# Performance work log

Hardware: AMD Instinct MI355X
Metric: run time of the kernel (lower is better)

Reference implementation:

```python
import jax, jax.numpy as jnp
import numpy as np

N_NODES = 50000
N_EDGES = 800000
IN_DIM, HID_DIM, EMB_DIM = 128, 256, 64


def setup_inputs() -> dict:
    key = jax.random.key(0)
    ks = jax.random.split(key, 10)
    x = jax.random.normal(ks[0], (N_NODES, IN_DIM), dtype=jnp.float32)
    edge_index = jax.random.randint(ks[1], (2, N_EDGES), 0, N_NODES, dtype=jnp.int64)
    def glorot(k, fan_in, fan_out):
        s = jnp.sqrt(6.0 / (fan_in + fan_out))
        return jax.random.uniform(k, (fan_in, fan_out), jnp.float32, -s, s)
    return {
        "x": x,
        "edge_index": edge_index,
        "W1": glorot(ks[2], IN_DIM, HID_DIM), "b1": jnp.zeros((HID_DIM,), jnp.float32),
        "W2": glorot(ks[3], HID_DIM, EMB_DIM), "b2": jnp.zeros((EMB_DIM,), jnp.float32),
        "W3": glorot(ks[4], EMB_DIM, HID_DIM), "b3": jnp.zeros((HID_DIM,), jnp.float32),
        "W4": glorot(ks[5], HID_DIM, IN_DIM), "b4": jnp.zeros((IN_DIM,), jnp.float32),
    }


def _gcn_conv(x, W, b, src, dst, norm, n_nodes):
    # linear transform, then edge gather -> normalize -> scatter-add (PyG GCNConv)
    h = x @ W                                    # [N, out]
    msg = h[src] * norm[:, None]                 # [E+N, out]
    out = jax.ops.segment_sum(msg, dst, num_segments=n_nodes)
    return out + b


def reference(x, edge_index, W1, b1, W2, b2, W3, b3, W4, b4):
    n = x.shape[0]
    loops = jnp.arange(n, dtype=edge_index.dtype)
    src = jnp.concatenate([edge_index[0], loops])  # add self-loops
    dst = jnp.concatenate([edge_index[1], loops])
    # symmetric degree normalization: deg computed on destination incl. self-loops
    deg = jax.ops.segment_sum(jnp.ones_like(dst, dtype=x.dtype), dst, num_segments=n)
    dis = jax.lax.rsqrt(jnp.maximum(deg, 1.0))
    norm = dis[src] * dis[dst]                   # [E+N]

    h = jax.nn.relu(_gcn_conv(x, W1, b1, src, dst, norm, n))
    h = jax.nn.relu(_gcn_conv(h, W2, b2, src, dst, norm, n))
    h = jax.nn.relu(_gcn_conv(h, W3, b3, src, dst, norm, n))
    out = _gcn_conv(h, W4, b4, src, dst, norm, n)
    return out
```

## Files before the change

### kernel.cpp

```cpp
#include <hip/hip_runtime.h>

#define N_NODES 50000
#define N_EDGES 800000

static inline size_t align256(size_t x) { return (x + 255) & ~(size_t)255; }

typedef _Float16 f16x8 __attribute__((ext_vector_type(8)));
typedef float f32x4 __attribute__((ext_vector_type(4)));
typedef float f32x8 __attribute__((ext_vector_type(8)));


__global__ void count_kernel(const int* __restrict__ dst, int* __restrict__ counts,
                             int* __restrict__ rank, int E) {
    int e = blockIdx.x * blockDim.x + threadIdx.x;
    if (e < E) rank[e] = atomicAdd(&counts[dst[e]], 1);
}

__global__ void scan1_kernel(const int* __restrict__ counts, int* __restrict__ row_ptr,
                             int* __restrict__ bsum, int n) {
    __shared__ int sd[1024];
    int i = blockIdx.x * 1024 + threadIdx.x;
    int v = (i < n) ? counts[i] : 0;
    sd[threadIdx.x] = v;
    __syncthreads();
    #pragma unroll
    for (int off = 1; off < 1024; off <<= 1) {
        int t = 0;
        if ((int)threadIdx.x >= off) t = sd[threadIdx.x - off];
        __syncthreads();
        sd[threadIdx.x] += t;
        __syncthreads();
    }
    if (i < n) row_ptr[i + 1] = sd[threadIdx.x];
    if (threadIdx.x == 1023) bsum[blockIdx.x] = sd[1023];
}

__global__ void scan3_kernel(int* __restrict__ row_ptr, const int* __restrict__ bsum,
                             const int* __restrict__ counts, float* __restrict__ dis, int n) {
    __shared__ int pfx_s;
    if (threadIdx.x == 0) {
        int nb = blockIdx.x >> 2;
        int p = 0;
        for (int j = 0; j < nb; ++j) p += bsum[j];
        pfx_s = p;
    }
    __syncthreads();
    int i = blockIdx.x * blockDim.x + threadIdx.x;
    if (i < n) {
        row_ptr[i + 1] += pfx_s;
        dis[i] = rsqrtf((float)(counts[i] + 1));
        if (i == 0) row_ptr[0] = 0;
    }
}

__global__ void fill_kernel(const int* __restrict__ src, const int* __restrict__ dst,
                            const int* __restrict__ rank, const int* __restrict__ row_ptr,
                            int* __restrict__ col, int E) {
    int e = blockIdx.x * blockDim.x + threadIdx.x;
    if (e < E) col[row_ptr[dst[e]] + rank[e]] = src[e];
}


__device__ __forceinline__ void pack_dev(const float* __restrict__ W,
                                         _Float16* __restrict__ Ph, _Float16* __restrict__ Pl,
                                         int K, int N, int id) {
    int l = id & 63;
    int f = id >> 6;
    int nf16 = N >> 4;
    int ks = f / nf16, nf = f - ks * nf16;
    int k0 = ks * 32 + (l >> 4) * 8;
    int n  = nf * 16 + (l & 15);
    #pragma unroll
    for (int j = 0; j < 8; ++j) {
        float v = W[(size_t)(k0 + j) * N + n];
        _Float16 hi = (_Float16)v;
        Ph[(size_t)id * 8 + j] = hi;
        Pl[(size_t)id * 8 + j] = (_Float16)(v - (float)hi);
    }
}

__global__ void prep_kernel(const float* __restrict__ W1, _Float16* __restrict__ w1h, _Float16* __restrict__ w1l,
                            const float* __restrict__ W2, _Float16* __restrict__ w2h, _Float16* __restrict__ w2l,
                            const float* __restrict__ W3, _Float16* __restrict__ w3h, _Float16* __restrict__ w3l,
                            const float* __restrict__ W4, _Float16* __restrict__ w4h, _Float16* __restrict__ w4l,
                            const float* __restrict__ x, const float* __restrict__ dis,
                            _Float16* __restrict__ xs) {
    int b = blockIdx.x;
    int tid = threadIdx.x;
    if (b < 16) {
        pack_dev(W1, w1h, w1l, 128, 256, b * 256 + tid);
    } else if (b < 24) {
        pack_dev(W2, w2h, w2l, 256, 64, (b - 16) * 256 + tid);
    } else if (b < 32) {
        pack_dev(W3, w3h, w3l, 64, 256, (b - 24) * 256 + tid);
    } else if (b < 48) {
        pack_dev(W4, w4h, w4l, 256, 128, (b - 32) * 256 + tid);
    } else {
        int q = (b - 48) * 256 + tid;
        if (q < N_NODES * 16) {
            int v = q >> 4, o = q & 15;
            float s = dis[v];
            const float* px = x + (size_t)v * 128 + o * 8;
            float4 t0 = *(const float4*)px;
            float4 t1 = *(const float4*)(px + 4);
            f16x8 h;
            h[0] = (_Float16)(s * t0.x); h[1] = (_Float16)(s * t0.y);
            h[2] = (_Float16)(s * t0.z); h[3] = (_Float16)(s * t0.w);
            h[4] = (_Float16)(s * t1.x); h[5] = (_Float16)(s * t1.y);
            h[6] = (_Float16)(s * t1.z); h[7] = (_Float16)(s * t1.w);
            ((f16x8*)xs)[q] = h;
        }
    }
}


template <int K1, int N2>
__global__ __launch_bounds__(256) void fused_gemm(
    const _Float16* __restrict__ Ah, const _Float16* __restrict__ Al,
    const float* __restrict__ dis, const float* __restrict__ bias1,
    const _Float16* __restrict__ B1h, const _Float16* __restrict__ B1l,
    const _Float16* __restrict__ B2h, const _Float16* __restrict__ B2l,
    _Float16* __restrict__ G16, int M) {

    constexpr int KS  = K1 / 32;
    constexpr int NF2 = N2 / 16;
    constexpr int NT2 = N2 / 64;
    constexpr int CS  = 16 / NF2;
    constexpr int KT2 = 8 / CS;

    __shared__ __align__(16) char ldsb[69632];
    f16x8* stg = (f16x8*)ldsb;

    const int t = threadIdx.x, w = t >> 6, l = t & 63;
    const int lrow = l & 15, lh = l >> 4;
    const int m0 = blockIdx.x * 64 + w * 16;
    const int v = m0 + lrow;
    const bool okv = v < M;

    f16x8 z8 = {0, 0, 0, 0, 0, 0, 0, 0};
    const f16x8* pAh = (const f16x8*)(Ah + (size_t)v * K1);
    const f16x8* pAl = (const f16x8*)(Al + (size_t)v * K1);
    f16x8 pah[KS], pal[KS];
    #pragma unroll
    for (int ks = 0; ks < KS; ++ks) {
        pah[ks] = okv ? pAh[ks * 4 + lh] : z8;
        pal[ks] = okv ? pAl[ks * 4 + lh] : z8;
    }

    const f16x8* b1h8 = (const f16x8*)B1h;
    const f16x8* b1l8 = (const f16x8*)B1l;
    f16x8 ph[4], pl[4];
    #pragma unroll
    for (int j = 0; j < 4; ++j) { ph[j] = b1h8[j * 256 + t]; pl[j] = b1l8[j * 256 + t]; }

    f32x4 acc1[4][4] = {};
    #pragma unroll
    for (int ks = 0; ks < KS; ++ks) {
        const int cur = ks & 1;
        #pragma unroll
        for (int j = 0; j < 4; ++j) {
            stg[(cur * 2 + 0) * 1024 + j * 256 + t] = ph[j];
            stg[(cur * 2 + 1) * 1024 + j * 256 + t] = pl[j];
        }
        if (ks + 1 < KS) {
            #pragma unroll
            for (int j = 0; j < 4; ++j) {
                ph[j] = b1h8[(size_t)(ks + 1) * 1024 + j * 256 + t];
                pl[j] = b1l8[(size_t)(ks + 1) * 1024 + j * 256 + t];
            }
        }
        __syncthreads();
        const f16x8* lbh = stg + (cur * 2 + 0) * 1024;
        const f16x8* lbl = stg + (cur * 2 + 1) * 1024;
        #pragma unroll
        for (int nt = 0; nt < 4; ++nt)
            #pragma unroll
            for (int c = 0; c < 4; ++c) {
                f16x8 bh = lbh[(nt * 4 + c) * 64 + l];
                f16x8 bl = lbl[(nt * 4 + c) * 64 + l];
                acc1[nt][c] = __builtin_amdgcn_mfma_f32_16x16x32_f16(pah[ks], bh, acc1[nt][c], 0, 0, 0);
                acc1[nt][c] = __builtin_amdgcn_mfma_f32_16x16x32_f16(pal[ks], bh, acc1[nt][c], 0, 0, 0);
                acc1[nt][c] = __builtin_amdgcn_mfma_f32_16x16x32_f16(pah[ks], bl, acc1[nt][c], 0, 0, 0);
            }
        __syncthreads();
    }

    float* xp = (float*)ldsb + (size_t)w * 4352;
    #pragma unroll
    for (int nt = 0; nt < 4; ++nt)
        #pragma unroll
        for (int c = 0; c < 4; ++c) {
            float bb = bias1[nt * 64 + c * 16 + lrow];
            #pragma unroll
            for (int r = 0; r < 4; ++r) {
                float hv = fmaxf(acc1[nt][c][r] + bb, 0.f);
                xp[(nt * 64 + c * 16 + lrow) * 17 + lh * 4 + r] = hv;
            }
        }

    const f16x8* b2h8 = (const f16x8*)B2h;
    const f16x8* b2l8 = (const f16x8*)B2l;
    #pragma unroll
    for (int j = 0; j < 4; ++j) { ph[j] = b2h8[j * 256 + t]; pl[j] = b2l8[j * 256 + t]; }

    f16x8 a2h[8], a2l[8];
    #pragma unroll
    for (int ks2 = 0; ks2 < 8; ++ks2)
        #pragma unroll
        for (int j = 0; j < 8; ++j) {
            float vv = xp[(ks2 * 32 + lh * 8 + j) * 17 + lrow];
            a2h[ks2][j] = (_Float16)vv;
            a2l[ks2][j] = (_Float16)(vv - (float)a2h[ks2][j]);
        }
    __syncthreads();

    f32x4 acc2[NT2][4] = {};
    #pragma unroll
    for (int kc = 0; kc < KT2; ++kc) {
        const int cur = kc & 1;
        #pragma unroll
        for (int j = 0; j < 4; ++j) {
            stg[(cur * 2 + 0) * 1024 + j * 256 + t] = ph[j];
            stg[(cur * 2 + 1) * 1024 + j * 256 + t] = pl[j];
        }
        if (kc + 1 < KT2) {
            #pragma unroll
            for (int j = 0; j < 4; ++j) {
                ph[j] = b2h8[(size_t)(kc + 1) * 1024 + j * 256 + t];
                pl[j] = b2l8[(size_t)(kc + 1) * 1024 + j * 256 + t];
            }
        }
        __syncthreads();
        const f16x8* lbh = stg + (cur * 2 + 0) * 1024;
        const f16x8* lbl = stg + (cur * 2 + 1) * 1024;
        #pragma unroll
        for (int cs = 0; cs < CS; ++cs) {
            const int ks2 = kc * CS + cs;
            #pragma unroll
            for (int nt2 = 0; nt2 < NT2; ++nt2)
                #pragma unroll
                for (int c = 0; c < 4; ++c) {
                    f16x8 bh = lbh[(cs * NF2 + nt2 * 4 + c) * 64 + l];
                    f16x8 bl = lbl[(cs * NF2 + nt2 * 4 + c) * 64 + l];
                    acc2[nt2][c] = __builtin_amdgcn_mfma_f32_16x16x32_f16(a2h[ks2], bh, acc2[nt2][c], 0, 0, 0);
                    acc2[nt2][c] = __builtin_amdgcn_mfma_f32_16x16x32_f16(a2l[ks2], bh, acc2[nt2][c], 0, 0, 0);
                    acc2[nt2][c] = __builtin_amdgcn_mfma_f32_16x16x32_f16(a2h[ks2], bl, acc2[nt2][c], 0, 0, 0);
                }
        }
        __syncthreads();
    }

    #pragma unroll
    for (int nt2 = 0; nt2 < NT2; ++nt2)
        #pragma unroll
        for (int r = 0; r < 4; ++r) {
            int m = m0 + lh * 4 + r;
            if (m < M) {
                float sc = dis[m];
                #pragma unroll
                for (int c = 0; c < 4; ++c)
                    G16[(size_t)m * N2 + nt2 * 64 + c * 16 + lrow] = (_Float16)(sc * acc2[nt2][c][r]);
            }
        }
}


template <int MODE, int DQ8>
__global__ __launch_bounds__(256) void agg8(
    const _Float16* __restrict__ g, const int* __restrict__ row_ptr,
    const int* __restrict__ col, const float* __restrict__ dis,
    const float* __restrict__ bias, float* __restrict__ outf,
    _Float16* __restrict__ o16, _Float16* __restrict__ oh, _Float16* __restrict__ ol) {
    const int NPB = 256 / DQ8;
    int t = threadIdx.x;
    int nl = t / DQ8, c = t % DQ8;
    int v = blockIdx.x * NPB + nl;
    if (v >= N_NODES) return;
    const f16x8* g8 = (const f16x8*)g;
    size_t rowo = (size_t)v * DQ8 + c;

    f32x8 sum = __builtin_convertvector(g8[rowo], f32x8);

    int s = row_ptr[v], e = row_ptr[v + 1];
    int i = s;
    for (; i + 4 <= e; i += 4) {
        int u0 = col[i], u1 = col[i + 1], u2 = col[i + 2], u3 = col[i + 3];
        f32x8 f0 = __builtin_convertvector(g8[(size_t)u0 * DQ8 + c], f32x8);
        f32x8 f1 = __builtin_convertvector(g8[(size_t)u1 * DQ8 + c], f32x8);
        f32x8 f2 = __builtin_convertvector(g8[(size_t)u2 * DQ8 + c], f32x8);
        f32x8 f3 = __builtin_convertvector(g8[(size_t)u3 * DQ8 + c], f32x8);
        sum += (f0 + f1) + (f2 + f3);
    }
    for (; i < e; ++i)
        sum += __builtin_convertvector(g8[(size_t)col[i] * DQ8 + c], f32x8);

    float dv = dis[v];
    if (MODE == 0) {
        f16x8 h, lo;
        #pragma unroll
        for (int j = 0; j < 8; ++j) {
            float r = dv * sum[j];
            h[j]  = (_Float16)r;
            lo[j] = (_Float16)(r - (float)h[j]);
        }
        ((f16x8*)oh)[rowo] = h;
        ((f16x8*)ol)[rowo] = lo;
    } else if (MODE == 2) {
        f32x8 bv = ((const f32x8*)bias)[c];
        f16x8 h;
        #pragma unroll
        for (int j = 0; j < 8; ++j) {
            float r = fmaxf(dv * sum[j] + bv[j], 0.f) * dv;
            h[j] = (_Float16)r;
        }
        ((f16x8*)o16)[rowo] = h;
    } else {
        f32x8 bv = ((const f32x8*)bias)[c];
        f32x8 r;
        #pragma unroll
        for (int j = 0; j < 8; ++j) r[j] = dv * sum[j] + bv[j];
        ((f32x8*)outf)[rowo] = r;
    }
}


extern "C" void kernel_launch(void* const* d_in, const int* in_sizes, int n_in,
                              void* d_out, int out_size, void* d_ws, size_t ws_size,
                              hipStream_t stream) {
    const int N = N_NODES, E = N_EDGES;

    const float* x   = (const float*)d_in[0];
    const int*   ei  = (const int*)d_in[1];
    const int*   src = ei;
    const int*   dst = ei + E;
    const float* W1 = (const float*)d_in[2];  const float* b1 = (const float*)d_in[3];
    const float* W2 = (const float*)d_in[4];  const float* b2 = (const float*)d_in[5];
    const float* W3 = (const float*)d_in[6];  const float* b3 = (const float*)d_in[7];
    const float* W4 = (const float*)d_in[8];  const float* b4 = (const float*)d_in[9];
    float* out = (float*)d_out;

    char* w = (char*)d_ws;
    int*   counts  = (int*)w;    w += align256((size_t)N * 4);
    int*   row_ptr = (int*)w;    w += align256((size_t)(N + 1) * 4);
    float* dis     = (float*)w;  w += align256((size_t)N * 4);
    int*   bsum    = (int*)w;    w += align256((size_t)64 * 4);
    int*   rank    = (int*)w;    w += align256((size_t)E * 4);
    int*   col     = (int*)w;    w += align256((size_t)E * 4);
    _Float16* w1h = (_Float16*)w; w += align256(32768 * 2);
    _Float16* w1l = (_Float16*)w; w += align256(32768 * 2);
    _Float16* w2h = (_Float16*)w; w += align256(16384 * 2);
    _Float16* w2l = (_Float16*)w; w += align256(16384 * 2);
    _Float16* w3h = (_Float16*)w; w += align256(16384 * 2);
    _Float16* w3l = (_Float16*)w; w += align256(16384 * 2);
    _Float16* w4h = (_Float16*)w; w += align256(32768 * 2);
    _Float16* w4l = (_Float16*)w; w += align256(32768 * 2);
    _Float16* xs  = (_Float16*)w; w += align256((size_t)N * 128 * 2);
    _Float16* t1h = (_Float16*)w; w += align256((size_t)N * 128 * 2);
    _Float16* t1l = (_Float16*)w; w += align256((size_t)N * 128 * 2);
    _Float16* g2  = (_Float16*)w; w += align256((size_t)N * 64 * 2);
    _Float16* h2s = (_Float16*)w; w += align256((size_t)N * 64 * 2);
    _Float16* t3h = (_Float16*)w; w += align256((size_t)N * 64 * 2);
    _Float16* t3l = (_Float16*)w; w += align256((size_t)N * 64 * 2);
    _Float16* gg4 = (_Float16*)w; w += align256((size_t)N * 128 * 2);

    const int nb = (N + 1023) / 1024;
    hipMemsetAsync(counts, 0, (size_t)N * 4, stream);
    count_kernel<<<(E + 255) / 256, 256, 0, stream>>>(dst, counts, rank, E);
    scan1_kernel<<<nb, 1024, 0, stream>>>(counts, row_ptr, bsum, N);
    scan3_kernel<<<(N + 255) / 256, 256, 0, stream>>>(row_ptr, bsum, counts, dis, N);
    fill_kernel<<<(E + 255) / 256, 256, 0, stream>>>(src, dst, rank, row_ptr, col, E);

    prep_kernel<<<48 + (N * 16 + 255) / 256, 256, 0, stream>>>(
        W1, w1h, w1l, W2, w2h, w2l, W3, w3h, w3l, W4, w4h, w4l, x, dis, xs);

    const int gx = (N + 63) / 64;

    agg8<0, 16><<<(N + 15) / 16, 256, 0, stream>>>(xs, row_ptr, col, dis, nullptr,
                                                   nullptr, nullptr, t1h, t1l);
    fused_gemm<128, 64><<<gx, 256, 0, stream>>>(t1h, t1l, dis, b1,
                                                w1h, w1l, w2h, w2l, g2, N);
    agg8<2, 8><<<(N + 31) / 32, 256, 0, stream>>>(g2, row_ptr, col, dis, b2,
                                                  nullptr, h2s, nullptr, nullptr);

    agg8<0, 8><<<(N + 31) / 32, 256, 0, stream>>>(h2s, row_ptr, col, dis, nullptr,
                                                  nullptr, nullptr, t3h, t3l);
    fused_gemm<64, 128><<<gx, 256, 0, stream>>>(t3h, t3l, dis, b3,
                                                w3h, w3l, w4h, w4l, gg4, N);
    agg8<3, 16><<<(N + 15) / 16, 256, 0, stream>>>(gg4, row_ptr, col, dis, b4,
                                                   out, nullptr, nullptr, nullptr);
}
```

Baseline: 224.4 us.

## Store gathered feature matrices in 32-column chunks and aggregate chunk by chunk

The fp16 feature buffers that get gathered (scaled input, GEMM outputs, layer-2 output) are now stored column-chunked: each 32-column slice of all nodes is contiguous. The aggregation kernel loops over chunks, with 4 threads per node each handling 8 columns. Within one pass, random neighbor gathers hit a smaller working set (50000 x 64 bytes) that is more likely to stay in L2/MALL. The cost is re-reading row_ptr and col once per chunk and fewer threads per node, which lowers parallelism per node.

```diff
diff --git a/kernel.cpp b/kernel.cpp
--- a/kernel.cpp
+++ b/kernel.cpp
@@ -108,7 +108,7 @@
             h[2] = (_Float16)(s * t0.z); h[3] = (_Float16)(s * t0.w);
             h[4] = (_Float16)(s * t1.x); h[5] = (_Float16)(s * t1.y);
             h[6] = (_Float16)(s * t1.z); h[7] = (_Float16)(s * t1.w);
-            ((f16x8*)xs)[q] = h;
+            ((f16x8*)xs)[(size_t)(o >> 2) * (N_NODES * 4) + (size_t)v * 4 + (o & 3)] = h;
         }
     }
 }
@@ -258,68 +258,74 @@
             if (m < M) {
                 float sc = dis[m];
                 #pragma unroll
-                for (int c = 0; c < 4; ++c)
-                    G16[(size_t)m * N2 + nt2 * 64 + c * 16 + lrow] = (_Float16)(sc * acc2[nt2][c][r]);
-            }
-        }
-}
-
-
-template <int MODE, int DQ8>
-__global__ __launch_bounds__(256) void agg8(
+                for (int c = 0; c < 4; ++c) {
+                    int n = nt2 * 64 + c * 16 + lrow;
+                    G16[(size_t)(n >> 5) * ((size_t)M * 32) + (size_t)m * 32 + (n & 31)] =
+                        (_Float16)(sc * acc2[nt2][c][r]);
+                }
+            }
+        }
+}
+
+
+template <int MODE, int OPR, int C>
+__global__ __launch_bounds__(256) void agg_chunk(
     const _Float16* __restrict__ g, const int* __restrict__ row_ptr,
     const int* __restrict__ col, const float* __restrict__ dis,
     const float* __restrict__ bias, float* __restrict__ outf,
     _Float16* __restrict__ o16, _Float16* __restrict__ oh, _Float16* __restrict__ ol) {
-    const int NPB = 256 / DQ8;
+
     int t = threadIdx.x;
-    int nl = t / DQ8, c = t % DQ8;
-    int v = blockIdx.x * NPB + nl;
+    int nl = t >> 2, c = t & 3;
+    int v = blockIdx.x * 64 + nl;
     if (v >= N_NODES) return;
-    const f16x8* g8 = (const f16x8*)g;
-    size_t rowo = (size_t)v * DQ8 + c;
-
-    f32x8 sum = __builtin_convertvector(g8[rowo], f32x8);
 
     int s = row_ptr[v], e = row_ptr[v + 1];
-    int i = s;
-    for (; i + 4 <= e; i += 4) {
-        int u0 = col[i], u1 = col[i + 1], u2 = col[i + 2], u3 = col[i + 3];
-        f32x8 f0 = __builtin_convertvector(g8[(size_t)u0 * DQ8 + c], f32x8);
-        f32x8 f1 = __builtin_convertvector(g8[(size_t)u1 * DQ8 + c], f32x8);
-        f32x8 f2 = __builtin_convertvector(g8[(size_t)u2 * DQ8 + c], f32x8);
-        f32x8 f3 = __builtin_convertvector(g8[(size_t)u3 * DQ8 + c], f32x8);
-        sum += (f0 + f1) + (f2 + f3);
-    }
-    for (; i < e; ++i)
-        sum += __builtin_convertvector(g8[(size_t)col[i] * DQ8 + c], f32x8);
-
     float dv = dis[v];
-    if (MODE == 0) {
-        f16x8 h, lo;
-        #pragma unroll
-        for (int j = 0; j < 8; ++j) {
-            float r = dv * sum[j];
-            h[j]  = (_Float16)r;
-            lo[j] = (_Float16)(r - (float)h[j]);
-        }
-        ((f16x8*)oh)[rowo] = h;
-        ((f16x8*)ol)[rowo] = lo;
-    } else if (MODE == 2) {
-        f32x8 bv = ((const f32x8*)bias)[c];
-        f16x8 h;
-        #pragma unroll
-        for (int j = 0; j < 8; ++j) {
-            float r = fmaxf(dv * sum[j] + bv[j], 0.f) * dv;
-            h[j] = (_Float16)r;
-        }
-        ((f16x8*)o16)[rowo] = h;
-    } else {
-        f32x8 bv = ((const f32x8*)bias)[c];
-        f32x8 r;
-        #pragma unroll
-        for (int j = 0; j < 8; ++j) r[j] = dv * sum[j] + bv[j];
-        ((f32x8*)outf)[rowo] = r;
+    const f16x8* gb = (const f16x8*)g;
+
+    #pragma unroll 1
+    for (int ch = 0; ch < C; ++ch) {
+        const f16x8* g8 = gb + (size_t)ch * (N_NODES * 4);
+        f32x8 sum = __builtin_convertvector(g8[(size_t)v * 4 + c], f32x8);
+        int i = s;
+        for (; i + 4 <= e; i += 4) {
+            int u0 = col[i], u1 = col[i + 1], u2 = col[i + 2], u3 = col[i + 3];
+            f32x8 f0 = __builtin_convertvector(g8[(size_t)u0 * 4 + c], f32x8);
+            f32x8 f1 = __builtin_convertvector(g8[(size_t)u1 * 4 + c], f32x8);
+            f32x8 f2 = __builtin_convertvector(g8[(size_t)u2 * 4 + c], f32x8);
+            f32x8 f3 = __builtin_convertvector(g8[(size_t)u3 * 4 + c], f32x8);
+            sum += (f0 + f1) + (f2 + f3);
+        }
+        for (; i < e; ++i)
+            sum += __builtin_convertvector(g8[(size_t)col[i] * 4 + c], f32x8);
+
+        if (MODE == 0) {
+            f16x8 h, lo;
+            #pragma unroll
+            for (int j = 0; j < 8; ++j) {
+                float r = dv * sum[j];
+                h[j]  = (_Float16)r;
+                lo[j] = (_Float16)(r - (float)h[j]);
+            }
+            ((f16x8*)oh)[(size_t)v * OPR + ch * 4 + c] = h;
+            ((f16x8*)ol)[(size_t)v * OPR + ch * 4 + c] = lo;
+        } else if (MODE == 2) {
+            f32x8 bv = ((const f32x8*)bias)[ch * 4 + c];
+            f16x8 h;
+            #pragma unroll
+            for (int j = 0; j < 8; ++j) {
+                float r = fmaxf(dv * sum[j] + bv[j], 0.f) * dv;
+                h[j] = (_Float16)r;
+            }
+            ((f16x8*)o16)[(size_t)ch * (N_NODES * 4) + (size_t)v * 4 + c] = h;
+        } else {
+            f32x8 bv = ((const f32x8*)bias)[ch * 4 + c];
+            f32x8 r;
+            #pragma unroll
+            for (int j = 0; j < 8; ++j) r[j] = dv * sum[j] + bv[j];
+            ((f32x8*)outf)[(size_t)v * (C * 4) + ch * 4 + c] = r;
+        }
     }
 }
 
@@ -373,19 +379,20 @@
     prep_kernel<<<48 + (N * 16 + 255) / 256, 256, 0, stream>>>(
         W1, w1h, w1l, W2, w2h, w2l, W3, w3h, w3l, W4, w4h, w4l, x, dis, xs);
 
+    const int ga = (N + 63) / 64;
     const int gx = (N + 63) / 64;
 
-    agg8<0, 16><<<(N + 15) / 16, 256, 0, stream>>>(xs, row_ptr, col, dis, nullptr,
-                                                   nullptr, nullptr, t1h, t1l);
+    agg_chunk<0, 16, 4><<<ga, 256, 0, stream>>>(xs, row_ptr, col, dis, nullptr,
+                                                nullptr, nullptr, t1h, t1l);
     fused_gemm<128, 64><<<gx, 256, 0, stream>>>(t1h, t1l, dis, b1,
                                                 w1h, w1l, w2h, w2l, g2, N);
-    agg8<2, 8><<<(N + 31) / 32, 256, 0, stream>>>(g2, row_ptr, col, dis, b2,
-                                                  nullptr, h2s, nullptr, nullptr);
-
-    agg8<0, 8><<<(N + 31) / 32, 256, 0, stream>>>(h2s, row_ptr, col, dis, nullptr,
-                                                  nullptr, nullptr, t3h, t3l);
+    agg_chunk<2, 0, 2><<<ga, 256, 0, stream>>>(g2, row_ptr, col, dis, b2,
+                                               nullptr, h2s, nullptr, nullptr);
+
+    agg_chunk<0, 8, 2><<<ga, 256, 0, stream>>>(h2s, row_ptr, col, dis, nullptr,
+                                               nullptr, nullptr, t3h, t3l);
     fused_gemm<64, 128><<<gx, 256, 0, stream>>>(t3h, t3l, dis, b3,
                                                 w3h, w3l, w4h, w4l, gg4, N);
-    agg8<3, 16><<<(N + 15) / 16, 256, 0, stream>>>(gg4, row_ptr, col, dis, b4,
-                                                   out, nullptr, nullptr, nullptr);
-}
+    agg_chunk<3, 0, 4><<<ga, 256, 0, stream>>>(gg4, row_ptr, col, dis, b4,
+                                               out, nullptr, nullptr, nullptr);
+}
```

Result: slower. 253.4 us (+12.9%).

## Stage CSR column indices in LDS for aggregation and drop per-iteration barriers

Applied to the files above, without the earlier changes.

The aggregation kernel now loads the block's contiguous range of neighbour indices into shared memory once, cooperatively and coalesced, and reads the indices from LDS in the gather loop instead of issuing repeated global loads per lane. If a block's edge range exceeds the buffer it falls back to the old global path. Separately, the trailing __syncthreads inside the double-buffered GEMM k-loops is removed or hoisted out of the loop to cut barrier overhead. Dropping that barrier risks a race where the next prefetch overwrites a staging buffer that other waves are still reading.

```diff
diff --git a/kernel.cpp b/kernel.cpp
--- a/kernel.cpp
+++ b/kernel.cpp
@@ -182,8 +182,8 @@
                 acc1[nt][c] = __builtin_amdgcn_mfma_f32_16x16x32_f16(pal[ks], bh, acc1[nt][c], 0, 0, 0);
                 acc1[nt][c] = __builtin_amdgcn_mfma_f32_16x16x32_f16(pah[ks], bl, acc1[nt][c], 0, 0, 0);
             }
-        __syncthreads();
-    }
+    }
+    __syncthreads();
 
     float* xp = (float*)ldsb + (size_t)w * 4352;
     #pragma unroll
@@ -247,7 +247,6 @@
                     acc2[nt2][c] = __builtin_amdgcn_mfma_f32_16x16x32_f16(a2h[ks2], bl, acc2[nt2][c], 0, 0, 0);
                 }
         }
-        __syncthreads();
     }
 
     #pragma unroll
@@ -271,28 +270,58 @@
     const int* __restrict__ col, const float* __restrict__ dis,
     const float* __restrict__ bias, float* __restrict__ outf,
     _Float16* __restrict__ o16, _Float16* __restrict__ oh, _Float16* __restrict__ ol) {
-    const int NPB = 256 / DQ8;
+    constexpr int NPB = 256 / DQ8;
+    constexpr int CAP = NPB * 64;
+    __shared__ int lcol[CAP];
+    __shared__ int sb2[2];
+
     int t = threadIdx.x;
+    int v0 = blockIdx.x * NPB;
+    int vend = v0 + NPB; if (vend > N_NODES) vend = N_NODES;
+    if (t == 0) { sb2[0] = row_ptr[v0]; sb2[1] = row_ptr[vend]; }
+    __syncthreads();
+    const int base = sb2[0];
+    const int tot  = sb2[1] - base;
+    const bool use_lds = (tot <= CAP);
+    if (use_lds) {
+        for (int j = t; j < tot; j += 256) lcol[j] = col[base + j];
+    }
+    __syncthreads();
+
     int nl = t / DQ8, c = t % DQ8;
-    int v = blockIdx.x * NPB + nl;
+    int v = v0 + nl;
     if (v >= N_NODES) return;
     const f16x8* g8 = (const f16x8*)g;
     size_t rowo = (size_t)v * DQ8 + c;
 
     f32x8 sum = __builtin_convertvector(g8[rowo], f32x8);
-
     int s = row_ptr[v], e = row_ptr[v + 1];
-    int i = s;
-    for (; i + 4 <= e; i += 4) {
-        int u0 = col[i], u1 = col[i + 1], u2 = col[i + 2], u3 = col[i + 3];
-        f32x8 f0 = __builtin_convertvector(g8[(size_t)u0 * DQ8 + c], f32x8);
-        f32x8 f1 = __builtin_convertvector(g8[(size_t)u1 * DQ8 + c], f32x8);
-        f32x8 f2 = __builtin_convertvector(g8[(size_t)u2 * DQ8 + c], f32x8);
-        f32x8 f3 = __builtin_convertvector(g8[(size_t)u3 * DQ8 + c], f32x8);
-        sum += (f0 + f1) + (f2 + f3);
-    }
-    for (; i < e; ++i)
-        sum += __builtin_convertvector(g8[(size_t)col[i] * DQ8 + c], f32x8);
+
+    if (use_lds) {
+        int i = s - base, en = e - base;
+        for (; i + 4 <= en; i += 4) {
+            int u0 = lcol[i], u1 = lcol[i + 1], u2 = lcol[i + 2], u3 = lcol[i + 3];
+            f32x8 f0 = __builtin_convertvector(g8[(size_t)u0 * DQ8 + c], f32x8);
+            f32x8 f1 = __builtin_convertvector(g8[(size_t)u1 * DQ8 + c], f32x8);
+            f32x8 f2 = __builtin_convertvector(g8[(size_t)u2 * DQ8 + c], f32x8);
+            f32x8 f3 = __builtin_convertvector(g8[(size_t)u3 * DQ8 + c], f32x8);
+            sum += (f0 + f1) + (f2 + f3);
+        }
+        for (; i < en; ++i)
+            sum += __builtin_convertvector(g8[(size_t)lcol[i] * DQ8 + c], f32x8);
+    } else {
+        int i = s;
+        for (; i + 4 <= e; i += 4) {
+            int u0 = col[i], u1 = col[i + 1], u2 = col[i + 2], u3 = col[i + 3];
+            f32x8 f0 = __builtin_convertvector(g8[(size_t)u0 * DQ8 + c], f32x8);
+            f32x8 f1 = __builtin_convertvector(g8[(size_t)u1 * DQ8 + c], f32x8);
+            f32x8 f2 = __builtin_convertvector(g8[(size_t)u2 * DQ8 + c], f32x8);
+            f32x8 f3 = __builtin_convertvector(g8[(size_t)u3 * DQ8 + c], f32x8);
+            sum += (f0 + f1) + (f2 + f3);
+        }
+        for (; i < e; ++i)
+            sum += __builtin_convertvector(g8[(size_t)col[i] * DQ8 + c], f32x8);
+    }
 
     float dv = dis[v];
     if (MODE == 0) {
```

Result: faster. 217.9 us (-2.9%).
